# Kernel optimization log

Measured on AMD Instinct MI355X. Metric: run time of the kernel, lower is better.

The kernel has to match this reference:

```python
import jax, jax.numpy as jnp
import numpy as np

EPS = 1e-5        # layer_norm_epsilon
N_HEAD = 16
PAD = 50257       # pad_token_id in select_at_last_token
L = 2             # len(layer_nums)


def _ln(x, g, b):
    m = jnp.mean(x, axis=-1, keepdims=True)
    v = jnp.mean(jnp.square(x - m), axis=-1, keepdims=True)
    return (x - m) * jax.lax.rsqrt(v + EPS) * g + b


def _attn_layer(hs, idx, g, b, Wq, Wk, Wv, Wo, bo):
    # hs: [B,S,D]; idx: [B] index of last non-pad token
    B, S, D = hs.shape
    hd = D // N_HEAD
    h = _ln(hs, g, b)
    last = h[jnp.arange(B), idx]                       # [B,D] select_at_last_token
    q = (last @ Wq).reshape(B, N_HEAD, hd)             # single query per sequence
    k = (h @ Wk).reshape(B, S, N_HEAD, hd)
    v = (h @ Wv).reshape(B, S, N_HEAD, hd)
    # GPT-Neo attention: NO 1/sqrt(head_dim) scaling; causal mask for the last
    # row (q_len=1, key_len=S) is all-ones so it is a no-op.
    scores = jnp.einsum('bhd,bshd->bhs', q, k)
    w = jax.nn.softmax(scores, axis=-1)
    o = jnp.einsum('bhs,bshd->bhd', w, v).reshape(B, D)
    return o @ Wo + bo


def setup_inputs() -> dict:
    key = jax.random.key(0)
    ks = jax.random.split(key, 12)
    B, S, D = 8, 2048, 2048
    Dc = L * D            # 4096, MLP input size
    I = 4 * Dc            # 16384, mlp_ratio * Dc
    s = 0.02
    return {
        'hs0': jax.random.normal(ks[0], (B, S, D), jnp.float32),
        'hs1': jax.random.normal(ks[1], (B, S, D), jnp.float32),
        'ids': jax.random.randint(ks[2], (B, S), 0, 50258),
        'ln_g': jnp.ones((L, D), jnp.float32),
        'ln_b': jnp.zeros((L, D), jnp.float32),
        'Wq': jax.random.normal(ks[3], (L, D, D), jnp.float32) * s,
        'Wk': jax.random.normal(ks[4], (L, D, D), jnp.float32) * s,
        'Wv': jax.random.normal(ks[5], (L, D, D), jnp.float32) * s,
        'Wo': jax.random.normal(ks[6], (L, D, D), jnp.float32) * s,
        'bo': jnp.zeros((L, D), jnp.float32),
        'W1': jax.random.normal(ks[7], (Dc, I), jnp.float32) * s,
        'b1': jnp.zeros((I,), jnp.float32),
        'W2': jax.random.normal(ks[8], (I, Dc), jnp.float32) * s,
        'b2': jnp.zeros((Dc,), jnp.float32),
        'Wl': jax.random.normal(ks[9], (Dc, 2), jnp.float32) * s,
        'bl': jnp.zeros((2,), jnp.float32),
    }


def reference(hs0, hs1, ids, ln_g, ln_b, Wq, Wk, Wv, Wo, bo, W1, b1, W2, b2, Wl, bl):
    # select_at_last_token index: argmax of cumsum of non-pad mask = last non-pad pos
    mask = (ids != PAD).astype(jnp.int32)
    idx = jnp.argmax(jnp.cumsum(mask, axis=1), axis=1)  # [B]
    hss = [hs0, hs1]
    attn_outs = [
        _attn_layer(hss[l], idx, ln_g[l], ln_b[l], Wq[l], Wk[l], Wv[l], Wo[l], bo[l])
        for l in range(L)
    ]
    h = jnp.concatenate(attn_outs, axis=-1)            # [B, L*D]
    m = jax.nn.gelu(h @ W1 + b1, approximate=False) @ W2 + b2
    h = h + m                                           # residual around MLP
    return h @ Wl + bl                                  # [B, 2] logits
```

## Files before the change

### kernel.cpp

```cpp
#include <hip/hip_runtime.h>
#include <math.h>

#define PAD_ID 50257
#define B_ 8
#define S_ 2048
#define D_ 2048
#define H_ 16
#define HD_ 128
#define L_ 2
#define DC_ 4096
#define I_ 16384
#define EPS_ 1e-5f

__device__ __forceinline__ int rfl(int x){ return __builtin_amdgcn_readfirstlane(x); }

__global__ __launch_bounds__(256) void kA(const int* __restrict__ ids, int* __restrict__ idx){
  int b = blockIdx.x, t = threadIdx.x;
  __shared__ int red[256];
  int best = -1;
  for (int s = t; s < S_; s += 256)
    if (ids[b*S_+s] != PAD_ID) best = s;
  red[t] = best; __syncthreads();
  for (int off=128; off; off>>=1){ if (t<off) red[t] = max(red[t], red[t+off]); __syncthreads(); }
  if (t==0) idx[b] = max(red[0], 0);
}

__global__ __launch_bounds__(256) void kA2(const float* __restrict__ hs0, const float* __restrict__ hs1,
                    const int* __restrict__ idx,
                    const float* __restrict__ g, const float* __restrict__ bt,
                    float* __restrict__ lnlT){
  int b = blockIdx.x, l = blockIdx.y, t = threadIdx.x;
  const float* hs = (l==0?hs0:hs1);
  const float* row = hs + ((size_t)b*S_ + idx[b])*D_;
  int d0 = t*8;
  float x[8]; float s=0.f, ss=0.f;
  #pragma unroll
  for(int k=0;k<8;k++){ x[k]=row[d0+k]; s+=x[k]; ss+=x[k]*x[k]; }
  __shared__ float r1[256], r2[256];
  r1[t]=s; r2[t]=ss; __syncthreads();
  for(int off=128; off; off>>=1){ if(t<off){ r1[t]+=r1[t+off]; r2[t]+=r2[t+off]; } __syncthreads(); }
  float m = r1[0]*(1.0f/D_); float var = r2[0]*(1.0f/D_) - m*m;
  float rstd = rsqrtf(var + EPS_);
  #pragma unroll
  for(int k=0;k<8;k++){
    int d = d0+k;
    lnlT[((size_t)l*D_ + d)*8 + b] = (x[k]-m)*rstd*g[l*D_+d] + bt[l*D_+d];
  }
}

__global__ __launch_bounds__(256) void gemv8(
    const float* __restrict__ W, const float* __restrict__ Xt, float* __restrict__ outAcc,
    int C, int N, int cs, long wStride, long xStride, long oStride){
  int t = threadIdx.x;
  int l = blockIdx.z;
  W += (size_t)l*wStride; Xt += (size_t)l*xStride; outAcc += (size_t)l*oStride;
  int lane = t & 63;
  int w = rfl(t >> 6);
  int cpw = C/(cs*4);
  int c0 = (blockIdx.y*4 + w)*cpw;
  float acc[8] = {0,0,0,0,0,0,0,0};
  const float* xp = Xt + (size_t)c0*8;
  const float* wp = W + (size_t)c0*N + (size_t)blockIdx.x*64 + lane;
  #pragma unroll 4
  for (int c=0; c<cpw; c++){
    float wv = wp[(size_t)c*N];
    #pragma unroll
    for(int r=0;r<8;r++) acc[r] += xp[c*8+r]*wv;
  }
  __shared__ float red[4][64][8];
  #pragma unroll
  for(int r=0;r<8;r++) red[w][lane][r] = acc[r];
  __syncthreads();
  if (t < 64){
    #pragma unroll
    for(int r=0;r<8;r++){
      float s = red[0][t][r]+red[1][t][r]+red[2][t][r]+red[3][t][r];
      atomicAdd(&outAcc[((size_t)blockIdx.x*64 + t)*8 + r], s);
    }
  }
}

__global__ __launch_bounds__(256) void kC(
    const float* __restrict__ Wk, const float* __restrict__ qT,
    const float* __restrict__ g, const float* __restrict__ bt,
    float* __restrict__ gqk, float* __restrict__ Sg, float* __restrict__ Sb){
  int t = threadIdx.x;
  int h = blockIdx.y; int l = blockIdx.z;
  int dp = blockIdx.x*256 + t;
  const float* wr = Wk + (size_t)l*D_*D_ + (size_t)dp*D_ + h*HD_;
  const float* qB = qT + ((size_t)l*D_ + h*HD_)*8;
  float a[8]={0,0,0,0,0,0,0,0};
  #pragma unroll 4
  for (int j4=0;j4<32;j4++){
    float4 wv = *(const float4*)(wr + j4*4);
    const float* qp = qB + j4*32;
    #pragma unroll
    for(int r=0;r<8;r++)
      a[r] += wv.x*qp[r] + wv.y*qp[8+r] + wv.z*qp[16+r] + wv.w*qp[24+r];
  }
  float gg = g[l*D_+dp], bb = bt[l*D_+dp];
  float sgl[8], sbl[8];
  #pragma unroll
  for(int r=0;r<8;r++){
    float gq = gg*a[r];
    gqk[((size_t)(l*8+r)*H_ + h)*D_ + dp] = gq;
    sgl[r] = gq;
    sbl[r] = bb*a[r];
  }
  __shared__ float red[256][8];
  #pragma unroll
  for(int r=0;r<8;r++) red[t][r]=sgl[r];
  __syncthreads();
  for(int off=128; off; off>>=1){ if(t<off){ for(int r=0;r<8;r++) red[t][r]+=red[t+off][r]; } __syncthreads(); }
  if (t<8) atomicAdd(&Sg[(l*8+t)*H_ + h], red[0][t]);
  __syncthreads();
  #pragma unroll
  for(int r=0;r<8;r++) red[t][r]=sbl[r];
  __syncthreads();
  for(int off=128; off; off>>=1){ if(t<off){ for(int r=0;r<8;r++) red[t][r]+=red[t+off][r]; } __syncthreads(); }
  if (t<8) atomicAdd(&Sb[(l*8+t)*H_ + h], red[0][t]);
}

__global__ __launch_bounds__(256) void kD(
    const float* __restrict__ hs0, const float* __restrict__ hs1,
    const float* __restrict__ gqk,
    float* __restrict__ accP, float* __restrict__ sumP, float* __restrict__ sqP){
  int t = threadIdx.x;
  int sc = blockIdx.x & 31, kh = blockIdx.x >> 5;
  int b = blockIdx.y, l = blockIdx.z;
  int lb = l*8 + b;
  const float* hs = (l==0?hs0:hs1) + (size_t)b*S_*D_;
  const float* gqp = gqk + (size_t)lb*H_*D_;
  int s0 = sc*64;
  int kb = kh*1024;
  __shared__ float smem[64*66 + 16*68];
  float* xT = smem;
  float* gT = smem + 64*66;
  int rq = t & 15, jg = t >> 4;
  int r0 = rq*4, jc = jg*4;
  float acc[4][16];
  #pragma unroll
  for(int rr=0;rr<4;rr++){
    #pragma unroll
    for(int h=0;h<16;h++) acc[rr][h]=0.f;
  }
  float sum[4]={0.f,0.f,0.f,0.f}, sq[4]={0.f,0.f,0.f,0.f};
  for (int c=0;c<16;c++){
    int cb = kb + c*64;
    #pragma unroll
    for (int q=0;q<4;q++){
      int fid = t + q*256;
      int row = fid >> 4, jo = (fid & 15)*4;
      float4 v = *(const float4*)(hs + (size_t)(s0+row)*D_ + cb + jo);
      float2* wp = (float2*)&xT[row*66 + jo];
      wp[0] = make_float2(v.x, v.y);
      wp[1] = make_float2(v.z, v.w);
    }
    {
      int hh = t >> 4, jo = (t & 15)*4;
      float4 gv = *(const float4*)(gqp + (size_t)hh*D_ + cb + jo);
      *(float4*)&gT[hh*68 + jo] = gv;
    }
    __syncthreads();
    float xv[4][4];
    #pragma unroll
    for (int rr=0;rr<4;rr++){
      const float2* xp = (const float2*)&xT[(r0+rr)*66 + jc];
      float2 xa = xp[0], xb = xp[1];
      xv[rr][0]=xa.x; xv[rr][1]=xa.y; xv[rr][2]=xb.x; xv[rr][3]=xb.y;
      sum[rr] += xa.x + xa.y + xb.x + xb.y;
      sq[rr]  += xa.x*xa.x + xa.y*xa.y + xb.x*xb.x + xb.y*xb.y;
    }
    #pragma unroll
    for (int h=0;h<16;h++){
      float4 gv = *(const float4*)&gT[h*68 + jc];
      #pragma unroll
      for (int rr=0;rr<4;rr++)
        acc[rr][h] += xv[rr][0]*gv.x + xv[rr][1]*gv.y + xv[rr][2]*gv.z + xv[rr][3]*gv.w;
    }
    __syncthreads();
  }
  #pragma unroll
  for (int rr=0;rr<4;rr++){
    #pragma unroll
    for (int h=0;h<16;h++){
      float v = acc[rr][h];
      v += __shfl_xor(v, 16);
      v += __shfl_xor(v, 32);
      acc[rr][h] = v;
    }
    float sv = sum[rr]; sv += __shfl_xor(sv, 16); sv += __shfl_xor(sv, 32); sum[rr] = sv;
    float qv = sq[rr];  qv += __shfl_xor(qv, 16); qv += __shfl_xor(qv, 32); sq[rr]  = qv;
  }
  __syncthreads();
  float* redL = smem;
  int w = t >> 6;
  if ((t & 63) < 16){
    float* p = &redL[(w*16 + rq)*73];
    #pragma unroll
    for (int rr=0;rr<4;rr++){
      #pragma unroll
      for (int h=0;h<16;h++) p[rr*16+h] = acc[rr][h];
      p[64+rr] = sum[rr];
      p[68+rr] = sq[rr];
    }
  }
  __syncthreads();
  if (t < 64){
    int frq = t >> 2, frr = t & 3;
    float ah[16];
    #pragma unroll
    for(int h=0;h<16;h++) ah[h]=0.f;
    float s1=0.f, s2=0.f;
    #pragma unroll
    for (int ww=0; ww<4; ww++){
      const float* p = &redL[(ww*16 + frq)*73];
      #pragma unroll
      for(int h=0;h<16;h++) ah[h] += p[frr*16+h];
      s1 += p[64+frr];
      s2 += p[68+frr];
    }
    int s = s0 + t;
    size_t base = (size_t)(kh*16 + lb)*16;
    #pragma unroll
    for(int h=0;h<16;h++)
      accP[(base + h)*S_ + s] = ah[h];
    sumP[(size_t)(kh*16+lb)*S_ + s] = s1;
    sqP[(size_t)(kh*16+lb)*S_ + s] = s2;
  }
}

__global__ __launch_bounds__(256) void kD2(
    const float* __restrict__ accP, const float* __restrict__ sumP, const float* __restrict__ sqP,
    const float* __restrict__ Sg, const float* __restrict__ Sb,
    float* __restrict__ scores, float* __restrict__ mu, float* __restrict__ rs){
  int t = threadIdx.x;
  int b = blockIdx.y, l = blockIdx.z;
  int lb = l*8 + b;
  int s = blockIdx.x*256 + t;
  float s1 = sumP[(size_t)lb*S_ + s] + sumP[(size_t)(16+lb)*S_ + s];
  float s2 = sqP[(size_t)lb*S_ + s]  + sqP[(size_t)(16+lb)*S_ + s];
  float m = s1*(1.0f/D_);
  float var = s2*(1.0f/D_) - m*m;
  float rst = rsqrtf(var + EPS_);
  mu[(size_t)lb*S_ + s] = m;
  rs[(size_t)lb*S_ + s] = rst;
  #pragma unroll
  for (int h=0;h<16;h++){
    float a = accP[((size_t)lb*16 + h)*S_ + s] + accP[((size_t)(16+lb)*16 + h)*S_ + s];
    scores[((size_t)lb*H_ + h)*S_ + s] = rst*(a - m*Sg[lb*H_+h]) + Sb[lb*H_+h];
  }
}

__global__ __launch_bounds__(256) void kE1(
    const float* __restrict__ scores, const float* __restrict__ mu, const float* __restrict__ rs,
    float* __restrict__ M, float* __restrict__ Sden, float* __restrict__ cc){
  int t=threadIdx.x; int h=blockIdx.x, b=blockIdx.y, l=blockIdx.z;
  int lb = l*8+b;
  const float* sc = scores + ((size_t)lb*H_ + h)*S_;
  __shared__ float red[256];
  __shared__ float red2[256];
  float mx = -1e30f;
  for (int s=t; s<S_; s+=256) mx = fmaxf(mx, sc[s]);
  red[t]=mx; __syncthreads();
  for(int off=128;off;off>>=1){ if(t<off) red[t]=fmaxf(red[t],red[t+off]); __syncthreads(); }
  float Mv = red[0];
  __syncthreads();
  float se=0.f, sce=0.f;
  const float* mup = mu + (size_t)lb*S_;
  const float* rsp = rs + (size_t)lb*S_;
  for (int s=t; s<S_; s+=256){
    float e = __expf(sc[s]-Mv);
    se += e;
    sce += e*rsp[s]*mup[s];
  }
  red[t]=se; red2[t]=sce; __syncthreads();
  for(int off=128;off;off>>=1){ if(t<off){red[t]+=red[t+off]; red2[t]+=red2[t+off];} __syncthreads(); }
  if(t==0){ M[lb*H_+h]=Mv; Sden[lb*H_+h]=red[0]; cc[lb*H_+h]=red2[0]/red[0]; }
}

__global__ __launch_bounds__(256) void kE2(
    const float* __restrict__ scores, const float* __restrict__ rs,
    const float* __restrict__ M, const float* __restrict__ Sden,
    float* __restrict__ u){
  int t=threadIdx.x; int scb=blockIdx.x, b=blockIdx.y, l=blockIdx.z;
  int lb=l*8+b;
  int lin0 = t*8;
  int sl = lin0 >> 4;
  int h0 = lin0 & 15;
  int s = scb*128 + sl;
  float rstv = rs[(size_t)lb*S_ + s];
  float out[8];
  #pragma unroll
  for(int k=0;k<8;k++){
    int h = h0 + k;
    float e = __expf(scores[((size_t)lb*H_+h)*S_ + s] - M[lb*H_+h]);
    out[k] = e / Sden[lb*H_+h] * rstv;
  }
  float* up = u + ((size_t)lb*S_ + s)*H_ + h0;
  *(float4*)up     = make_float4(out[0],out[1],out[2],out[3]);
  *(float4*)(up+4) = make_float4(out[4],out[5],out[6],out[7]);
}

__global__ __launch_bounds__(256) void kF(
    const float* __restrict__ hs0, const float* __restrict__ hs1,
    const float* __restrict__ u, float* __restrict__ Fpart){
  int t=threadIdx.x;
  int sc = blockIdx.x>>2, dq = blockIdx.x&3;
  int b=blockIdx.y, l=blockIdx.z;
  int lb=l*8+b;
  const float* hs = (l==0?hs0:hs1) + (size_t)b*S_*D_;
  int d0 = dq*512 + t*2;
  float acc[16][2];
  #pragma unroll
  for(int h=0;h<16;h++){ acc[h][0]=0.f; acc[h][1]=0.f; }
  int s0 = sc*128;
  #pragma unroll 4
  for (int si=0; si<128; si++){
    int s = s0+si;
    const float* up = u + ((size_t)lb*S_ + s)*H_;
    float4 u0 = *(const float4*)up, u1 = *(const float4*)(up+4),
           u2 = *(const float4*)(up+8), u3 = *(const float4*)(up+12);
    float uu[16] = {u0.x,u0.y,u0.z,u0.w, u1.x,u1.y,u1.z,u1.w,
                    u2.x,u2.y,u2.z,u2.w, u3.x,u3.y,u3.z,u3.w};
    float2 x = *(const float2*)(hs + (size_t)s*D_ + d0);
    #pragma unroll
    for(int h=0;h<16;h++){ acc[h][0] += uu[h]*x.x; acc[h][1] += uu[h]*x.y; }
  }
  #pragma unroll
  for(int h=0;h<16;h++)
    *(float2*)(Fpart + (((size_t)lb*16 + sc)*H_ + h)*D_ + d0) = make_float2(acc[h][0], acc[h][1]);
}

__global__ __launch_bounds__(256) void kF2(
    const float* __restrict__ Fpart, const float* __restrict__ g, float* __restrict__ gAT){
  int n = blockIdx.x*256 + threadIdx.x;
  int d = n & (D_-1);
  int h = (n >> 11) & 15;
  int l = n >> 15;
  float gg = g[l*D_+d];
  float out[8];
  #pragma unroll
  for(int b=0;b<8;b++){
    float s=0.f;
    for(int scn=0;scn<16;scn++)
      s += Fpart[(((size_t)(l*8+b)*16 + scn)*H_ + h)*D_ + d];
    out[b]=gg*s;
  }
  float* op = gAT + (size_t)n*8;
  *(float4*)op     = make_float4(out[0],out[1],out[2],out[3]);
  *(float4*)(op+4) = make_float4(out[4],out[5],out[6],out[7]);
}

__global__ __launch_bounds__(256) void kG(
    const float* __restrict__ Wv, const float* __restrict__ gAT,
    const float* __restrict__ g, const float* __restrict__ bt,
    float* __restrict__ Opart){
  int t=threadIdx.x;
  int d4=blockIdx.x, h=blockIdx.y, l=blockIdx.z;
  int j = t & 127;
  int dg = rfl(t >> 7);
  const float* wv = Wv + (size_t)l*D_*D_ + h*HD_ + j;
  const float* gA = gAT + ((size_t)l*H_ + h)*D_*8;
  float acc[8]={0,0,0,0,0,0,0,0}; float ag=0.f, ab=0.f;
  int dstart = d4*256 + dg*128;
  #pragma unroll 2
  for (int dd=0; dd<128; dd++){
    int d = dstart+dd;
    float wvv = wv[(size_t)d*D_];
    const float* xa = gA + (size_t)d*8;
    #pragma unroll
    for(int r=0;r<8;r++) acc[r] += xa[r]*wvv;
    ag += g[l*D_+d]*wvv;
    ab += bt[l*D_+d]*wvv;
  }
  __shared__ float red[2][128][10];
  float* p = red[dg][j];
  #pragma unroll
  for(int r=0;r<8;r++) p[r]=acc[r];
  p[8]=ag; p[9]=ab;
  __syncthreads();
  if (t<128){
    const float* q0=red[0][t]; const float* q1=red[1][t];
    #pragma unroll
    for(int r=0;r<10;r++)
      atomicAdd(&Opart[(((size_t)l*H_+h)*HD_ + t)*10 + r], q0[r]+q1[r]);
  }
}

__global__ void kG2(const float* __restrict__ Opart, const float* __restrict__ cc,
                    float* __restrict__ oT){
  int n = blockIdx.x*256 + threadIdx.x;
  int j = n & 127; int h = (n>>7) & 15; int l = n>>11;
  const float* p = Opart + (size_t)n*10;
  float ag=p[8], ab=p[9];
  #pragma unroll
  for(int b=0;b<8;b++){
    float c = cc[(l*8+b)*H_+h];
    oT[((size_t)l*D_ + h*HD_ + j)*8 + b] = p[b] - c*ag + ab;
  }
}

__global__ void kInitH(const float* __restrict__ bo, float* __restrict__ hcatT){
  int n = blockIdx.x*256 + threadIdx.x;
  hcatT[n] = bo[n>>3];
}

__global__ void kH2(float* __restrict__ t1T, const float* __restrict__ b1){
  int i = blockIdx.x*256 + threadIdx.x;
  float bv = b1[i];
  float* p = t1T + (size_t)i*8;
  #pragma unroll
  for(int k=0;k<8;k++){
    float x = p[k] + bv;
    p[k] = 0.5f*x*(1.0f + erff(x*0.70710678118654752440f));
  }
}

__global__ void kH2b(const float* __restrict__ hcatT, const float* __restrict__ b2, float* __restrict__ h2T){
  int j = blockIdx.x*256 + threadIdx.x;
  float bv = b2[j];
  #pragma unroll
  for(int k=0;k<8;k++) h2T[(size_t)j*8+k] = hcatT[(size_t)j*8+k] + bv;
}

__global__ __launch_bounds__(256) void kH4(const float* __restrict__ h2T, const float* __restrict__ Wl,
                    const float* __restrict__ bl, float* __restrict__ out){
  int t=threadIdx.x;
  float acc[8][2];
  #pragma unroll
  for(int b=0;b<8;b++){acc[b][0]=0.f;acc[b][1]=0.f;}
  for (int j=t; j<DC_; j+=256){
    float w0=Wl[j*2], w1=Wl[j*2+1];
    const float* hp = h2T + (size_t)j*8;
    #pragma unroll
    for(int b=0;b<8;b++){ float x=hp[b]; acc[b][0]+=x*w0; acc[b][1]+=x*w1; }
  }
  __shared__ float red[256][16];
  #pragma unroll
  for(int b=0;b<8;b++){ red[t][b*2]=acc[b][0]; red[t][b*2+1]=acc[b][1]; }
  __syncthreads();
  for(int off=128;off;off>>=1){ if(t<off){ for(int k=0;k<16;k++) red[t][k]+=red[t+off][k]; } __syncthreads(); }
  if (t<16) out[t] = red[0][t] + bl[t&1];
}

extern "C" void kernel_launch(void* const* d_in, const int* in_sizes, int n_in,
                              void* d_out, int out_size, void* d_ws, size_t ws_size,
                              hipStream_t stream) {
  (void)in_sizes; (void)n_in; (void)out_size;
  const float* hs0 = (const float*)d_in[0];
  const float* hs1 = (const float*)d_in[1];
  const int*   ids = (const int*)d_in[2];
  const float* ln_g = (const float*)d_in[3];
  const float* ln_b = (const float*)d_in[4];
  const float* Wq = (const float*)d_in[5];
  const float* Wk = (const float*)d_in[6];
  const float* Wv = (const float*)d_in[7];
  const float* Wo = (const float*)d_in[8];
  const float* bo = (const float*)d_in[9];
  const float* W1 = (const float*)d_in[10];
  const float* b1 = (const float*)d_in[11];
  const float* W2 = (const float*)d_in[12];
  const float* b2 = (const float*)d_in[13];
  const float* Wl = (const float*)d_in[14];
  const float* bl = (const float*)d_in[15];
  float* out = (float*)d_out;
  float* ws = (float*)d_ws;

  size_t o = 0;
  int* idx = (int*)ws;        o += 16;
  float* qT = ws + o;         o += (size_t)L_*D_*8;
  float* Sg = ws + o;         o += 256;
  float* Sb = ws + o;         o += 256;
  float* Opart = ws + o;      o += (size_t)L_*H_*HD_*10;
  float* t1T = ws + o;        o += (size_t)I_*8;
  size_t atomicFloats = o - 16;
  float* lnlT = ws + o;       o += (size_t)L_*D_*8;
  float* gqk = ws + o;        o += (size_t)L_*8*H_*D_;
  float* mu = ws + o;         o += (size_t)L_*8*S_;
  float* rs_ = ws + o;        o += (size_t)L_*8*S_;
  float* scores = ws + o;     o += (size_t)L_*8*H_*S_;
  float* M = ws + o;          o += 256;
  float* Sden = ws + o;       o += 256;
  float* cc = ws + o;         o += 256;
  float* u = ws + o;          o += (size_t)L_*8*S_*H_;
  float* Fpart = ws + o;      o += (size_t)L_*8*16*H_*D_;
  float* gAT = ws + o;        o += (size_t)L_*H_*D_*8;
  float* oT = ws + o;         o += (size_t)L_*D_*8;
  float* hcatT = ws + o;      o += (size_t)DC_*8;
  float* h2T = ws + o;        o += (size_t)DC_*8;
  if (o*4 > ws_size) return;

  float* accP = Fpart;
  float* sumP = Fpart + (size_t)2*16*16*2048;
  float* sqP  = sumP + (size_t)2*16*2048;

  hipMemsetAsync((void*)(ws + 16), 0, atomicFloats*4, stream);

  kA<<<8,256,0,stream>>>(ids, idx);
  kA2<<<dim3(8,2),256,0,stream>>>(hs0,hs1,idx,ln_g,ln_b,lnlT);
  gemv8<<<dim3(32,8,2),256,0,stream>>>(Wq, lnlT, qT, D_, D_, 8,
                                       (long)D_*D_, (long)D_*8, (long)D_*8);
  kC<<<dim3(8,16,2),256,0,stream>>>(Wk, qT, ln_g, ln_b, gqk, Sg, Sb);
  kD<<<dim3(64,8,2),256,0,stream>>>(hs0,hs1,gqk,accP,sumP,sqP);
  kD2<<<dim3(8,8,2),256,0,stream>>>(accP,sumP,sqP,Sg,Sb,scores,mu,rs_);
  kE1<<<dim3(16,8,2),256,0,stream>>>(scores,mu,rs_,M,Sden,cc);
  kE2<<<dim3(16,8,2),256,0,stream>>>(scores,rs_,M,Sden,u);
  kF<<<dim3(64,8,2),256,0,stream>>>(hs0,hs1,u,Fpart);
  kF2<<<256,256,0,stream>>>(Fpart, ln_g, gAT);
  kG<<<dim3(8,16,2),256,0,stream>>>(Wv, gAT, ln_g, ln_b, Opart);
  kG2<<<16,256,0,stream>>>(Opart, cc, oT);
  kInitH<<<128,256,0,stream>>>(bo, hcatT);
  gemv8<<<dim3(32,8,2),256,0,stream>>>(Wo, oT, hcatT, D_, D_, 8,
                                       (long)D_*D_, (long)D_*8, (long)D_*8);
  gemv8<<<dim3(256,4,1),256,0,stream>>>(W1, hcatT, t1T, DC_, I_, 4, 0,0,0);
  kH2<<<64,256,0,stream>>>(t1T, b1);
  kH2b<<<16,256,0,stream>>>(hcatT, b2, h2T);
  gemv8<<<dim3(64,16,1),256,0,stream>>>(W2, t1T, h2T, I_, DC_, 16, 0,0,0);
  kH4<<<1,256,0,stream>>>(h2T, Wl, bl, out);
}
```

Before: 1.016 ms.

## Fuse small kernels, split softmax stats, swizzle kD smem, widen GEMV splits

Merges the last-token index search into the layernorm-row kernel and folds the softmax max into kD2 via per-block partial maxima. Exp-sum and weighted-mean reductions move into kE2 with atomics, and the denominator division is deferred to kF2 and kG2i, which removes the separate kE1 pass. kD now splits K into four 512-wide chunks with an XOR-swizzled shared tile instead of padding. The GEMV launches gain more K-splits and unroll, several elementwise kernels are fused, and the final projection runs across 8 blocks with atomics. The cost is more atomics, more partial buffers to reduce, and extra memsets, including zeroing the output.

```diff
diff --git a/kernel.cpp b/kernel.cpp
--- a/kernel.cpp
+++ b/kernel.cpp
@@ -14,24 +14,20 @@
 
 __device__ __forceinline__ int rfl(int x){ return __builtin_amdgcn_readfirstlane(x); }
 
-__global__ __launch_bounds__(256) void kA(const int* __restrict__ ids, int* __restrict__ idx){
-  int b = blockIdx.x, t = threadIdx.x;
-  __shared__ int red[256];
+__global__ __launch_bounds__(256) void kAB(const float* __restrict__ hs0, const float* __restrict__ hs1,
+                    const int* __restrict__ ids,
+                    const float* __restrict__ g, const float* __restrict__ bt,
+                    float* __restrict__ lnlT){
+  int b = blockIdx.x, l = blockIdx.y, t = threadIdx.x;
+  __shared__ int redi[256];
   int best = -1;
   for (int s = t; s < S_; s += 256)
     if (ids[b*S_+s] != PAD_ID) best = s;
-  red[t] = best; __syncthreads();
-  for (int off=128; off; off>>=1){ if (t<off) red[t] = max(red[t], red[t+off]); __syncthreads(); }
-  if (t==0) idx[b] = max(red[0], 0);
-}
-
-__global__ __launch_bounds__(256) void kA2(const float* __restrict__ hs0, const float* __restrict__ hs1,
-                    const int* __restrict__ idx,
-                    const float* __restrict__ g, const float* __restrict__ bt,
-                    float* __restrict__ lnlT){
-  int b = blockIdx.x, l = blockIdx.y, t = threadIdx.x;
+  redi[t] = best; __syncthreads();
+  for (int off=128; off; off>>=1){ if (t<off) redi[t] = max(redi[t], redi[t+off]); __syncthreads(); }
+  int ix = max(redi[0], 0);
   const float* hs = (l==0?hs0:hs1);
-  const float* row = hs + ((size_t)b*S_ + idx[b])*D_;
+  const float* row = hs + ((size_t)b*S_ + ix)*D_;
   int d0 = t*8;
   float x[8]; float s=0.f, ss=0.f;
   #pragma unroll
@@ -61,7 +57,7 @@
   float acc[8] = {0,0,0,0,0,0,0,0};
   const float* xp = Xt + (size_t)c0*8;
   const float* wp = W + (size_t)c0*N + (size_t)blockIdx.x*64 + lane;
-  #pragma unroll 4
+  #pragma unroll 8
   for (int c=0; c<cpw; c++){
     float wv = wp[(size_t)c*N];
     #pragma unroll
@@ -132,12 +128,12 @@
   const float* hs = (l==0?hs0:hs1) + (size_t)b*S_*D_;
   const float* gqp = gqk + (size_t)lb*H_*D_;
   int s0 = sc*64;
-  int kb = kh*1024;
-  __shared__ float smem[64*66 + 16*68];
+  int kb = kh*512;
+  __shared__ float smem[64*64 + 16*68];
   float* xT = smem;
-  float* gT = smem + 64*66;
+  float* gT = smem + 64*64;
   int rq = t & 15, jg = t >> 4;
-  int r0 = rq*4, jc = jg*4;
+  int r0 = rq*4;
   float acc[4][16];
   #pragma unroll
   for(int rr=0;rr<4;rr++){
@@ -145,16 +141,14 @@
     for(int h=0;h<16;h++) acc[rr][h]=0.f;
   }
   float sum[4]={0.f,0.f,0.f,0.f}, sq[4]={0.f,0.f,0.f,0.f};
-  for (int c=0;c<16;c++){
+  for (int c=0;c<8;c++){
     int cb = kb + c*64;
     #pragma unroll
     for (int q=0;q<4;q++){
       int fid = t + q*256;
-      int row = fid >> 4, jo = (fid & 15)*4;
-      float4 v = *(const float4*)(hs + (size_t)(s0+row)*D_ + cb + jo);
-      float2* wp = (float2*)&xT[row*66 + jo];
-      wp[0] = make_float2(v.x, v.y);
-      wp[1] = make_float2(v.z, v.w);
+      int row = fid >> 4, jo4 = fid & 15;
+      float4 v = *(const float4*)(hs + (size_t)(s0+row)*D_ + cb + jo4*4);
+      *(float4*)&xT[(row<<6) + ((jo4 ^ (row&7))<<2)] = v;
     }
     {
       int hh = t >> 4, jo = (t & 15)*4;
@@ -165,15 +159,15 @@
     float xv[4][4];
     #pragma unroll
     for (int rr=0;rr<4;rr++){
-      const float2* xp = (const float2*)&xT[(r0+rr)*66 + jc];
-      float2 xa = xp[0], xb = xp[1];
-      xv[rr][0]=xa.x; xv[rr][1]=xa.y; xv[rr][2]=xb.x; xv[rr][3]=xb.y;
-      sum[rr] += xa.x + xa.y + xb.x + xb.y;
-      sq[rr]  += xa.x*xa.x + xa.y*xa.y + xb.x*xb.x + xb.y*xb.y;
+      int row = r0+rr;
+      float4 x4 = *(const float4*)&xT[(row<<6) + ((jg ^ (row&7))<<2)];
+      xv[rr][0]=x4.x; xv[rr][1]=x4.y; xv[rr][2]=x4.z; xv[rr][3]=x4.w;
+      sum[rr] += x4.x + x4.y + x4.z + x4.w;
+      sq[rr]  += x4.x*x4.x + x4.y*x4.y + x4.z*x4.z + x4.w*x4.w;
     }
     #pragma unroll
     for (int h=0;h<16;h++){
-      float4 gv = *(const float4*)&gT[h*68 + jc];
+      float4 gv = *(const float4*)&gT[h*68 + jg*4];
       #pragma unroll
       for (int rr=0;rr<4;rr++)
         acc[rr][h] += xv[rr][0]*gv.x + xv[rr][1]*gv.y + xv[rr][2]*gv.z + xv[rr][3]*gv.w;
@@ -233,73 +227,99 @@
 __global__ __launch_bounds__(256) void kD2(
     const float* __restrict__ accP, const float* __restrict__ sumP, const float* __restrict__ sqP,
     const float* __restrict__ Sg, const float* __restrict__ Sb,
-    float* __restrict__ scores, float* __restrict__ mu, float* __restrict__ rs){
+    float* __restrict__ scores, float* __restrict__ mu, float* __restrict__ rs,
+    float* __restrict__ PM){
   int t = threadIdx.x;
   int b = blockIdx.y, l = blockIdx.z;
   int lb = l*8 + b;
   int s = blockIdx.x*256 + t;
-  float s1 = sumP[(size_t)lb*S_ + s] + sumP[(size_t)(16+lb)*S_ + s];
-  float s2 = sqP[(size_t)lb*S_ + s]  + sqP[(size_t)(16+lb)*S_ + s];
+  float s1 = 0.f, s2 = 0.f;
+  #pragma unroll
+  for (int kh=0; kh<4; kh++){
+    s1 += sumP[(size_t)(kh*16+lb)*S_ + s];
+    s2 += sqP[(size_t)(kh*16+lb)*S_ + s];
+  }
   float m = s1*(1.0f/D_);
   float var = s2*(1.0f/D_) - m*m;
   float rst = rsqrtf(var + EPS_);
   mu[(size_t)lb*S_ + s] = m;
   rs[(size_t)lb*S_ + s] = rst;
+  __shared__ float redm[256][17];
   #pragma unroll
   for (int h=0;h<16;h++){
-    float a = accP[((size_t)lb*16 + h)*S_ + s] + accP[((size_t)(16+lb)*16 + h)*S_ + s];
-    scores[((size_t)lb*H_ + h)*S_ + s] = rst*(a - m*Sg[lb*H_+h]) + Sb[lb*H_+h];
-  }
-}
-
-__global__ __launch_bounds__(256) void kE1(
-    const float* __restrict__ scores, const float* __restrict__ mu, const float* __restrict__ rs,
-    float* __restrict__ M, float* __restrict__ Sden, float* __restrict__ cc){
-  int t=threadIdx.x; int h=blockIdx.x, b=blockIdx.y, l=blockIdx.z;
-  int lb = l*8+b;
-  const float* sc = scores + ((size_t)lb*H_ + h)*S_;
-  __shared__ float red[256];
-  __shared__ float red2[256];
-  float mx = -1e30f;
-  for (int s=t; s<S_; s+=256) mx = fmaxf(mx, sc[s]);
-  red[t]=mx; __syncthreads();
-  for(int off=128;off;off>>=1){ if(t<off) red[t]=fmaxf(red[t],red[t+off]); __syncthreads(); }
-  float Mv = red[0];
-  __syncthreads();
-  float se=0.f, sce=0.f;
-  const float* mup = mu + (size_t)lb*S_;
-  const float* rsp = rs + (size_t)lb*S_;
-  for (int s=t; s<S_; s+=256){
-    float e = __expf(sc[s]-Mv);
-    se += e;
-    sce += e*rsp[s]*mup[s];
-  }
-  red[t]=se; red2[t]=sce; __syncthreads();
-  for(int off=128;off;off>>=1){ if(t<off){red[t]+=red[t+off]; red2[t]+=red2[t+off];} __syncthreads(); }
-  if(t==0){ M[lb*H_+h]=Mv; Sden[lb*H_+h]=red[0]; cc[lb*H_+h]=red2[0]/red[0]; }
+    float a = 0.f;
+    #pragma unroll
+    for (int kh=0; kh<4; kh++)
+      a += accP[((size_t)(kh*16+lb)*16 + h)*S_ + s];
+    float scv = rst*(a - m*Sg[lb*H_+h]) + Sb[lb*H_+h];
+    scores[((size_t)lb*H_ + h)*S_ + s] = scv;
+    redm[t][h] = scv;
+  }
+  __syncthreads();
+  for(int off=128;off;off>>=1){
+    if(t<off){
+      #pragma unroll
+      for(int h=0;h<16;h++) redm[t][h] = fmaxf(redm[t][h], redm[t+off][h]);
+    }
+    __syncthreads();
+  }
+  if (t<16) PM[(lb*H_ + t)*8 + blockIdx.x] = redm[0][t];
 }
 
 __global__ __launch_bounds__(256) void kE2(
-    const float* __restrict__ scores, const float* __restrict__ rs,
-    const float* __restrict__ M, const float* __restrict__ Sden,
-    float* __restrict__ u){
+    const float* __restrict__ scores, const float* __restrict__ rs, const float* __restrict__ mu,
+    const float* __restrict__ PM,
+    float* __restrict__ u, float* __restrict__ SdenP, float* __restrict__ SceP){
   int t=threadIdx.x; int scb=blockIdx.x, b=blockIdx.y, l=blockIdx.z;
   int lb=l*8+b;
-  int lin0 = t*8;
-  int sl = lin0 >> 4;
-  int h0 = lin0 & 15;
+  __shared__ float Mh[16];
+  if (t < 16){
+    float m = -1e30f;
+    #pragma unroll
+    for (int sb=0; sb<8; sb++) m = fmaxf(m, PM[(lb*H_ + t)*8 + sb]);
+    Mh[t] = m;
+  }
+  __syncthreads();
+  int sl = t >> 1;
+  int h0 = (t & 1)*8;
   int s = scb*128 + sl;
   float rstv = rs[(size_t)lb*S_ + s];
+  float muv  = mu[(size_t)lb*S_ + s];
   float out[8];
+  __shared__ float se[256][9], sce[256][9];
   #pragma unroll
   for(int k=0;k<8;k++){
     int h = h0 + k;
-    float e = __expf(scores[((size_t)lb*H_+h)*S_ + s] - M[lb*H_+h]);
-    out[k] = e / Sden[lb*H_+h] * rstv;
+    float e = __expf(scores[((size_t)lb*H_+h)*S_ + s] - Mh[h]);
+    out[k] = e * rstv;
+    se[t][k] = e;
+    sce[t][k] = e * rstv * muv;
   }
   float* up = u + ((size_t)lb*S_ + s)*H_ + h0;
   *(float4*)up     = make_float4(out[0],out[1],out[2],out[3]);
   *(float4*)(up+4) = make_float4(out[4],out[5],out[6],out[7]);
+  __syncthreads();
+  for(int off=128; off>=2; off>>=1){
+    if(t<off){
+      #pragma unroll
+      for(int k=0;k<8;k++){ se[t][k]+=se[t+off][k]; sce[t][k]+=sce[t+off][k]; }
+    }
+    __syncthreads();
+  }
+  if (t==0){
+    #pragma unroll
+    for(int k=0;k<8;k++){
+      atomicAdd(&SdenP[lb*H_ + k], se[0][k]);
+      atomicAdd(&SceP[lb*H_ + k], sce[0][k]);
+    }
+  }
+  if (t==1){
+    #pragma unroll
+    for(int k=0;k<8;k++){
+      atomicAdd(&SdenP[lb*H_ + 8 + k], se[1][k]);
+      atomicAdd(&SceP[lb*H_ + 8 + k], sce[1][k]);
+    }
+  }
 }
 
 __global__ __launch_bounds__(256) void kF(
@@ -333,7 +353,8 @@
 }
 
 __global__ __launch_bounds__(256) void kF2(
-    const float* __restrict__ Fpart, const float* __restrict__ g, float* __restrict__ gAT){
+    const float* __restrict__ Fpart, const float* __restrict__ g,
+    const float* __restrict__ SdenP, float* __restrict__ gAT){
   int n = blockIdx.x*256 + threadIdx.x;
   int d = n & (D_-1);
   int h = (n >> 11) & 15;
@@ -345,7 +366,7 @@
     float s=0.f;
     for(int scn=0;scn<16;scn++)
       s += Fpart[(((size_t)(l*8+b)*16 + scn)*H_ + h)*D_ + d];
-    out[b]=gg*s;
+    out[b] = gg*s/SdenP[(l*8+b)*H_ + h];
   }
   float* op = gAT + (size_t)n*8;
   *(float4*)op     = make_float4(out[0],out[1],out[2],out[3]);
@@ -388,49 +409,58 @@
   }
 }
 
-__global__ void kG2(const float* __restrict__ Opart, const float* __restrict__ cc,
-                    float* __restrict__ oT){
+__global__ __launch_bounds__(256) void kG2i(const float* __restrict__ Opart,
+                    const float* __restrict__ SdenP, const float* __restrict__ SceP,
+                    const float* __restrict__ bo,
+                    float* __restrict__ oT, float* __restrict__ hcatT){
   int n = blockIdx.x*256 + threadIdx.x;
-  int j = n & 127; int h = (n>>7) & 15; int l = n>>11;
-  const float* p = Opart + (size_t)n*10;
-  float ag=p[8], ab=p[9];
-  #pragma unroll
-  for(int b=0;b<8;b++){
-    float c = cc[(l*8+b)*H_+h];
-    oT[((size_t)l*D_ + h*HD_ + j)*8 + b] = p[b] - c*ag + ab;
-  }
-}
-
-__global__ void kInitH(const float* __restrict__ bo, float* __restrict__ hcatT){
-  int n = blockIdx.x*256 + threadIdx.x;
-  hcatT[n] = bo[n>>3];
-}
-
-__global__ void kH2(float* __restrict__ t1T, const float* __restrict__ b1){
-  int i = blockIdx.x*256 + threadIdx.x;
-  float bv = b1[i];
-  float* p = t1T + (size_t)i*8;
-  #pragma unroll
-  for(int k=0;k<8;k++){
-    float x = p[k] + bv;
-    p[k] = 0.5f*x*(1.0f + erff(x*0.70710678118654752440f));
-  }
-}
-
-__global__ void kH2b(const float* __restrict__ hcatT, const float* __restrict__ b2, float* __restrict__ h2T){
-  int j = blockIdx.x*256 + threadIdx.x;
-  float bv = b2[j];
-  #pragma unroll
-  for(int k=0;k<8;k++) h2T[(size_t)j*8+k] = hcatT[(size_t)j*8+k] + bv;
+  if (n < 4096){
+    int j = n & 127; int h = (n>>7) & 15; int l = n>>11;
+    const float* p = Opart + (size_t)n*10;
+    float ag=p[8], ab=p[9];
+    #pragma unroll
+    for(int b=0;b<8;b++){
+      int lb = l*8+b;
+      float c = SceP[lb*H_+h] / SdenP[lb*H_+h];
+      oT[((size_t)l*D_ + h*HD_ + j)*8 + b] = p[b] - c*ag + ab;
+    }
+  } else {
+    int m = n - 4096;
+    hcatT[m] = bo[m>>3];
+  }
+}
+
+__global__ __launch_bounds__(256) void kH2f(float* __restrict__ t1T, const float* __restrict__ b1,
+                    const float* __restrict__ hcatT, const float* __restrict__ b2,
+                    float* __restrict__ h2T){
+  int bx = blockIdx.x, t = threadIdx.x;
+  if (bx < 64){
+    int i = bx*256 + t;
+    float bv = b1[i];
+    float* p = t1T + (size_t)i*8;
+    #pragma unroll
+    for(int k=0;k<8;k++){
+      float x = p[k] + bv;
+      p[k] = 0.5f*x*(1.0f + erff(x*0.70710678118654752440f));
+    }
+  } else {
+    int j = (bx-64)*256 + t;
+    float bv = b2[j];
+    #pragma unroll
+    for(int k=0;k<8;k++) h2T[(size_t)j*8+k] = hcatT[(size_t)j*8+k] + bv;
+  }
 }
 
 __global__ __launch_bounds__(256) void kH4(const float* __restrict__ h2T, const float* __restrict__ Wl,
                     const float* __restrict__ bl, float* __restrict__ out){
-  int t=threadIdx.x;
+  int t=threadIdx.x, bx=blockIdx.x;
   float acc[8][2];
   #pragma unroll
   for(int b=0;b<8;b++){acc[b][0]=0.f;acc[b][1]=0.f;}
-  for (int j=t; j<DC_; j+=256){
+  int j0 = bx*512;
+  #pragma unroll
+  for (int jj=0; jj<2; jj++){
+    int j = j0 + jj*256 + t;
     float w0=Wl[j*2], w1=Wl[j*2+1];
     const float* hp = h2T + (size_t)j*8;
     #pragma unroll
@@ -441,7 +471,7 @@
   for(int b=0;b<8;b++){ red[t][b*2]=acc[b][0]; red[t][b*2+1]=acc[b][1]; }
   __syncthreads();
   for(int off=128;off;off>>=1){ if(t<off){ for(int k=0;k<16;k++) red[t][k]+=red[t+off][k]; } __syncthreads(); }
-  if (t<16) out[t] = red[0][t] + bl[t&1];
+  if (t<16) atomicAdd(&out[t], red[0][t] + (bx==0 ? bl[t&1] : 0.f));
 }
 
 extern "C" void kernel_launch(void* const* d_in, const int* in_sizes, int n_in,
@@ -468,21 +498,21 @@
   float* ws = (float*)d_ws;
 
   size_t o = 0;
-  int* idx = (int*)ws;        o += 16;
+  o += 16;
   float* qT = ws + o;         o += (size_t)L_*D_*8;
   float* Sg = ws + o;         o += 256;
   float* Sb = ws + o;         o += 256;
   float* Opart = ws + o;      o += (size_t)L_*H_*HD_*10;
   float* t1T = ws + o;        o += (size_t)I_*8;
+  float* SdenP = ws + o;      o += 256;
+  float* SceP = ws + o;       o += 256;
   size_t atomicFloats = o - 16;
   float* lnlT = ws + o;       o += (size_t)L_*D_*8;
   float* gqk = ws + o;        o += (size_t)L_*8*H_*D_;
   float* mu = ws + o;         o += (size_t)L_*8*S_;
   float* rs_ = ws + o;        o += (size_t)L_*8*S_;
   float* scores = ws + o;     o += (size_t)L_*8*H_*S_;
-  float* M = ws + o;          o += 256;
-  float* Sden = ws + o;       o += 256;
-  float* cc = ws + o;         o += 256;
+  float* PM = ws + o;         o += 2048;
   float* u = ws + o;          o += (size_t)L_*8*S_*H_;
   float* Fpart = ws + o;      o += (size_t)L_*8*16*H_*D_;
   float* gAT = ws + o;        o += (size_t)L_*H_*D_*8;
@@ -492,30 +522,27 @@
   if (o*4 > ws_size) return;
 
   float* accP = Fpart;
-  float* sumP = Fpart + (size_t)2*16*16*2048;
-  float* sqP  = sumP + (size_t)2*16*2048;
+  float* sumP = Fpart + (size_t)4*16*16*2048;
+  float* sqP  = sumP + (size_t)4*16*2048;
 
   hipMemsetAsync((void*)(ws + 16), 0, atomicFloats*4, stream);
-
-  kA<<<8,256,0,stream>>>(ids, idx);
-  kA2<<<dim3(8,2),256,0,stream>>>(hs0,hs1,idx,ln_g,ln_b,lnlT);
+  hipMemsetAsync((void*)out, 0, 16*4, stream);
+
+  kAB<<<dim3(8,2),256,0,stream>>>(hs0,hs1,ids,ln_g,ln_b,lnlT);
   gemv8<<<dim3(32,8,2),256,0,stream>>>(Wq, lnlT, qT, D_, D_, 8,
                                        (long)D_*D_, (long)D_*8, (long)D_*8);
   kC<<<dim3(8,16,2),256,0,stream>>>(Wk, qT, ln_g, ln_b, gqk, Sg, Sb);
-  kD<<<dim3(64,8,2),256,0,stream>>>(hs0,hs1,gqk,accP,sumP,sqP);
-  kD2<<<dim3(8,8,2),256,0,stream>>>(accP,sumP,sqP,Sg,Sb,scores,mu,rs_);
-  kE1<<<dim3(16,8,2),256,0,stream>>>(scores,mu,rs_,M,Sden,cc);
-  kE2<<<dim3(16,8,2),256,0,stream>>>(scores,rs_,M,Sden,u);
+  kD<<<dim3(128,8,2),256,0,stream>>>(hs0,hs1,gqk,accP,sumP,sqP);
+  kD2<<<dim3(8,8,2),256,0,stream>>>(accP,sumP,sqP,Sg,Sb,scores,mu,rs_,PM);
+  kE2<<<dim3(16,8,2),256,0,stream>>>(scores,rs_,mu,PM,u,SdenP,SceP);
   kF<<<dim3(64,8,2),256,0,stream>>>(hs0,hs1,u,Fpart);
-  kF2<<<256,256,0,stream>>>(Fpart, ln_g, gAT);
+  kF2<<<256,256,0,stream>>>(Fpart, ln_g, SdenP, gAT);
   kG<<<dim3(8,16,2),256,0,stream>>>(Wv, gAT, ln_g, ln_b, Opart);
-  kG2<<<16,256,0,stream>>>(Opart, cc, oT);
-  kInitH<<<128,256,0,stream>>>(bo, hcatT);
+  kG2i<<<144,256,0,stream>>>(Opart, SdenP, SceP, bo, oT, hcatT);
   gemv8<<<dim3(32,8,2),256,0,stream>>>(Wo, oT, hcatT, D_, D_, 8,
                                        (long)D_*D_, (long)D_*8, (long)D_*8);
-  gemv8<<<dim3(256,4,1),256,0,stream>>>(W1, hcatT, t1T, DC_, I_, 4, 0,0,0);
-  kH2<<<64,256,0,stream>>>(t1T, b1);
-  kH2b<<<16,256,0,stream>>>(hcatT, b2, h2T);
-  gemv8<<<dim3(64,16,1),256,0,stream>>>(W2, t1T, h2T, I_, DC_, 16, 0,0,0);
-  kH4<<<1,256,0,stream>>>(h2T, Wl, bl, out);
-}
+  gemv8<<<dim3(256,8,1),256,0,stream>>>(W1, hcatT, t1T, DC_, I_, 8, 0,0,0);
+  kH2f<<<80,256,0,stream>>>(t1T, b1, hcatT, b2, h2T);
+  gemv8<<<dim3(64,32,1),256,0,stream>>>(W2, t1T, h2T, I_, DC_, 32, 0,0,0);
+  kH4<<<8,256,0,stream>>>(h2T, Wl, bl, out);
+}
```

After: 983.3 us. 1.03x faster.
